# Kernel tuning notes

Hardware: AMD Instinct MI355X
Metric: run time of the kernel (lower is better)

Reference implementation:

```python
import jax, jax.numpy as jnp
import numpy as np

DELTA_V = 0.5
DELTA_D = 1.5
ALPHA = 1.0
BETA = 1.0
GAMMA = 0.001
K = 33  # segment count: id 0 = background, 1..32 = instances (matches fill_max)


def setup_inputs() -> dict:
    key = jax.random.key(0)
    k1, k2 = jax.random.split(key)
    embeddings = jax.random.normal(k1, (8, 16, 512, 512), dtype=jnp.float32)
    instance_masks = jax.random.randint(k2, (8, 512, 512), 0, K, dtype=jnp.int32)
    return {"embeddings": embeddings, "instance_masks": instance_masks}


def _safe_norm(sq):
    # sqrt with zero-safe gradient: returns 0 where sq == 0
    pos = sq > 0
    return jnp.sqrt(jnp.where(pos, sq, 1.0)) * pos.astype(sq.dtype)


def _per_image(emb, mask):
    # emb: (E, H, W), mask: (H, W)
    E = emb.shape[0]
    emb_flat = emb.reshape(E, -1).T            # (N, E)
    ids = mask.reshape(-1)                      # (N,)

    counts = jax.ops.segment_sum(jnp.ones(ids.shape, jnp.float32), ids, num_segments=K)  # (K,)
    sums = jax.ops.segment_sum(emb_flat, ids, num_segments=K)                             # (K, E)
    counts_c = jnp.maximum(counts, 1.0)
    means = sums / counts_c[:, None]            # (K, E)

    present = counts[1:] > 0                    # (K-1,) which instance ids appear
    n_inst = present.sum().astype(jnp.float32)

    # variance (pull) term: per-pixel distance to own instance mean
    diff = emb_flat - means[ids]                # (N, E)
    pix_d = _safe_norm(jnp.sum(diff * diff, axis=1))
    var_term = jnp.maximum(pix_d - DELTA_V, 0.0) ** 2
    var_per = jax.ops.segment_sum(var_term, ids, num_segments=K)[1:]  # drop background seg
    var_loss = jnp.sum(jnp.where(present, var_per / counts_c[1:], 0.0)) / jnp.maximum(n_inst, 1.0)

    # distance (push) term: pairwise centroid distances among present instances
    m = means[1:]                               # (K-1, E)
    dsq = jnp.sum((m[:, None, :] - m[None, :, :]) ** 2, axis=-1)
    dmat = _safe_norm(dsq)
    pair_mask = (jnp.triu(jnp.ones((K - 1, K - 1), bool), 1)
                 & present[:, None] & present[None, :])
    n_pairs = pair_mask.sum().astype(jnp.float32)
    dist_term = jnp.maximum(2.0 * DELTA_D - dmat, 0.0) ** 2
    dist_loss = jnp.sum(jnp.where(pair_mask, dist_term, 0.0)) / jnp.maximum(n_pairs, 1.0)
    dist_loss = dist_loss * (n_inst > 1.0).astype(jnp.float32)

    # regularization: mean centroid norm over present instances
    mean_norms = _safe_norm(jnp.sum(m * m, axis=1))
    reg_loss = jnp.sum(jnp.where(present, mean_norms, 0.0)) / jnp.maximum(n_inst, 1.0)

    valid = (n_inst > 0.0).astype(jnp.float32)
    return var_loss * valid, dist_loss * valid, reg_loss * valid, valid


def reference(embeddings, instance_masks):
    v, d, r, valid = jax.vmap(_per_image)(embeddings, instance_masks)
    vs = jnp.maximum(valid.sum(), 1.0)
    var_loss = v.sum() / vs
    dist_loss = d.sum() / vs
    reg_loss = r.sum() / vs
    total = ALPHA * var_loss + BETA * dist_loss + GAMMA * reg_loss
    return jnp.stack([total, var_loss, dist_loss, reg_loss])
```

## Files before the change

kernel.cpp:

```cpp
#include <hip/hip_runtime.h>
#include <math.h>


#define B 8
#define E 16
#define HW (512*512)
#define BLK 256
#define P1_BPI 128
#define P2_BPI 64
#define P2_VPB (HW / 4 / P2_BPI)

typedef __attribute__((ext_vector_type(8)))  short short8;
typedef __attribute__((ext_vector_type(16))) float floatx16;

__device__ __forceinline__ float atomAddF(float* p, float v) {
  return unsafeAtomicAdd(p, v);
}

__device__ __forceinline__ short f2bf(float f) {
  unsigned u = __float_as_uint(f);
  u = u + 0x7FFF + ((u >> 16) & 1);
  return (short)(u >> 16);
}

__global__ __launch_bounds__(BLK) void pass1_kernel(
    const float* __restrict__ emb, const int* __restrict__ mask,
    float* __restrict__ gsum ) {
  __shared__ float lred[4][32][33];
  const int b    = blockIdx.y;
  const int t    = threadIdx.x;
  const int lane = t & 63;
  const int wv   = __builtin_amdgcn_readfirstlane(t >> 6);
  const int n    = lane & 31;
  const int h    = lane >> 5;
  const int myid = n + 1;

  const int ppw    = HW / (P1_BPI * 4);
  const int base   = (blockIdx.x * 4 + wv) * ppw;
  const int ntiles = ppw / 16;

  const int*   __restrict__ mb = mask + (size_t)b * HW + base;
  const float* __restrict__ pl = emb + ((size_t)b * E + (n & 15)) * HW + base + 8 * h;

  floatx16 acc;
#pragma unroll
  for (int i = 0; i < 16; ++i) acc[i] = 0.f;

#pragma unroll 2
  for (int tl = 0; tl < ntiles; ++tl) {
    const int4 m0 = ((const int4*)(mb + tl * 16))[0];
    const int4 m1 = ((const int4*)(mb + tl * 16))[1];
    const int4 m2 = ((const int4*)(mb + tl * 16))[2];
    const int4 m3 = ((const int4*)(mb + tl * 16))[3];

    short8 bf;
    if (n < 16) {
      const float4 f0 = ((const float4*)(pl + tl * 16))[0];
      const float4 f1 = ((const float4*)(pl + tl * 16))[1];
      bf[0] = f2bf(f0.x); bf[1] = f2bf(f0.y); bf[2] = f2bf(f0.z); bf[3] = f2bf(f0.w);
      bf[4] = f2bf(f1.x); bf[5] = f2bf(f1.y); bf[6] = f2bf(f1.z); bf[7] = f2bf(f1.w);
    } else if (n == 16) {
      const short one = (short)0x3F80;
      bf[0]=one; bf[1]=one; bf[2]=one; bf[3]=one; bf[4]=one; bf[5]=one; bf[6]=one; bf[7]=one;
    } else {
      bf[0]=0; bf[1]=0; bf[2]=0; bf[3]=0; bf[4]=0; bf[5]=0; bf[6]=0; bf[7]=0;
    }

    const int4 ma = h ? m2 : m0;
    const int4 mc = h ? m3 : m1;
    short8 af;
    af[0] = (ma.x == myid) ? (short)0x3F80 : (short)0;
    af[1] = (ma.y == myid) ? (short)0x3F80 : (short)0;
    af[2] = (ma.z == myid) ? (short)0x3F80 : (short)0;
    af[3] = (ma.w == myid) ? (short)0x3F80 : (short)0;
    af[4] = (mc.x == myid) ? (short)0x3F80 : (short)0;
    af[5] = (mc.y == myid) ? (short)0x3F80 : (short)0;
    af[6] = (mc.z == myid) ? (short)0x3F80 : (short)0;
    af[7] = (mc.w == myid) ? (short)0x3F80 : (short)0;

    acc = __builtin_amdgcn_mfma_f32_32x32x16_bf16(af, bf, acc, 0, 0, 0);
  }

#pragma unroll
  for (int r = 0; r < 16; ++r) {
    const int row = (r & 3) + 8 * (r >> 2) + 4 * h;
    lred[wv][row][n] = acc[r];
  }
  __syncthreads();

  for (int i = t; i < 32 * 32; i += BLK) {
    const int row = i >> 5, col = i & 31;
    if (col < 17) {
      const float s = lred[0][row][col] + lred[1][row][col]
                    + lred[2][row][col] + lred[3][row][col];
      atomAddF(&gsum[((size_t)b * 32 + row) * 17 + col], s);
    }
  }
}

__global__ __launch_bounds__(BLK) void pass2_kernel(
    const float* __restrict__ emb, const int* __restrict__ mask,
    const float* __restrict__ gsum, float* __restrict__ var_per ) {
  __shared__ float mean[33][20];
  __shared__ float slots[4][64][33];
  const int b    = blockIdx.y;
  const int t    = threadIdx.x;
  const int lane = t & 63;
  const int wv   = t >> 6;

  for (int i = t; i < 33 * 20; i += BLK) {
    const int k = i / 20, e = i - k * 20;
    float m = 0.f;
    if (k >= 1 && e < E) {
      const float c  = gsum[((size_t)b * 32 + (k - 1)) * 17 + 16];
      const float cc = c > 1.f ? c : 1.f;
      m = gsum[((size_t)b * 32 + (k - 1)) * 17 + e] / cc;
    }
    mean[k][e] = m;
  }
  for (int i = t; i < 4 * 64 * 33; i += BLK) (&slots[0][0][0])[i] = 0.f;
  __syncthreads();

  const int4*  __restrict__ maskv = (const int4*)(mask + (size_t)b * HW);
  const float* __restrict__ embb  = emb + (size_t)b * E * HW;
  float* mys = &slots[wv][lane][0];
  const int v0 = blockIdx.x * P2_VPB;

#pragma unroll 1
  for (int v = v0 + t; v < v0 + P2_VPB; v += BLK) {
    const int4 id = maskv[v];
    float d0 = 0.f, d1 = 0.f, d2 = 0.f, d3 = 0.f;
#pragma unroll
    for (int j = 0; j < 4; ++j) {
      const float4 x0 = ((const float4*)(embb + (size_t)(4 * j + 0) * HW))[v];
      const float4 x1 = ((const float4*)(embb + (size_t)(4 * j + 1) * HW))[v];
      const float4 x2 = ((const float4*)(embb + (size_t)(4 * j + 2) * HW))[v];
      const float4 x3 = ((const float4*)(embb + (size_t)(4 * j + 3) * HW))[v];
      const float4 m0 = *(const float4*)&mean[id.x][4 * j];
      const float4 m1 = *(const float4*)&mean[id.y][4 * j];
      const float4 m2 = *(const float4*)&mean[id.z][4 * j];
      const float4 m3 = *(const float4*)&mean[id.w][4 * j];
      float u;
      u = x0.x - m0.x; d0 += u * u;  u = x1.x - m0.y; d0 += u * u;
      u = x2.x - m0.z; d0 += u * u;  u = x3.x - m0.w; d0 += u * u;
      u = x0.y - m1.x; d1 += u * u;  u = x1.y - m1.y; d1 += u * u;
      u = x2.y - m1.z; d1 += u * u;  u = x3.y - m1.w; d1 += u * u;
      u = x0.z - m2.x; d2 += u * u;  u = x1.z - m2.y; d2 += u * u;
      u = x2.z - m2.z; d2 += u * u;  u = x3.z - m2.w; d2 += u * u;
      u = x0.w - m3.x; d3 += u * u;  u = x1.w - m3.y; d3 += u * u;
      u = x2.w - m3.z; d3 += u * u;  u = x3.w - m3.w; d3 += u * u;
    }
    float hh;
    hh = fmaxf(sqrtf(d0) - 0.5f, 0.f); mys[id.x] += hh * hh;
    hh = fmaxf(sqrtf(d1) - 0.5f, 0.f); mys[id.y] += hh * hh;
    hh = fmaxf(sqrtf(d2) - 0.5f, 0.f); mys[id.z] += hh * hh;
    hh = fmaxf(sqrtf(d3) - 0.5f, 0.f); mys[id.w] += hh * hh;
  }
  __syncthreads();

  for (int i = t; i < 64 * 33; i += BLK) {
    const int l = i / 33, k = i - l * 33;
    slots[0][l][k] += slots[1][l][k] + slots[2][l][k] + slots[3][l][k];
  }
  __syncthreads();
  if (t >= 1 && t < 33) {
    float s = 0.f;
    for (int l = 0; l < 64; ++l) s += slots[0][l][t];
    atomAddF(&var_per[b * 32 + (t - 1)], s);
  }
}

__global__ __launch_bounds__(BLK) void final_kernel(
    const float* __restrict__ gsum, const float* __restrict__ var_per,
    float* __restrict__ out) {
  __shared__ float mean[B][32][E];
  __shared__ float cnts[B][32];
  __shared__ float vb[B], rb[B], db[B], pb[B], nb[B];
  const int t = threadIdx.x;

  if (t < B) { vb[t] = 0.f; rb[t] = 0.f; db[t] = 0.f; pb[t] = 0.f; nb[t] = 0.f; }
  {
    const int bb = t >> 5, k = t & 31;
    const float c  = gsum[((size_t)bb * 32 + k) * 17 + 16];
    const float cc = c > 1.f ? c : 1.f;
    cnts[bb][k] = c;
#pragma unroll
    for (int e = 0; e < E; ++e)
      mean[bb][k][e] = gsum[((size_t)bb * 32 + k) * 17 + e] / cc;
  }
  __syncthreads();

  {
    const int bb = t >> 5, k = t & 31;
    const float c = cnts[bb][k];
    if (c > 0.5f) {
      atomAddF(&nb[bb], 1.f);
      atomAddF(&vb[bb], var_per[bb * 32 + k] / c);
      float sq = 0.f;
#pragma unroll
      for (int e = 0; e < E; ++e) { const float m = mean[bb][k][e]; sq += m * m; }
      atomAddF(&rb[bb], sq > 0.f ? sqrtf(sq) : 0.f);
    }
  }
  __syncthreads();

  for (int idx = t; idx < B * 32 * 32; idx += BLK) {
    const int bb = idx >> 10;
    const int p  = idx & 1023;
    const int i  = p >> 5;
    const int j  = p & 31;
    if (i < j && cnts[bb][i] > 0.5f && cnts[bb][j] > 0.5f) {
      atomAddF(&pb[bb], 1.f);
      float sq = 0.f;
#pragma unroll
      for (int e = 0; e < E; ++e) {
        const float d = mean[bb][i][e] - mean[bb][j][e];
        sq += d * d;
      }
      const float dn = sq > 0.f ? sqrtf(sq) : 0.f;
      const float hh = 3.0f - dn;
      if (hh > 0.f) atomAddF(&db[bb], hh * hh);
    }
  }
  __syncthreads();

  if (t == 0) {
    float sv = 0.f, sd = 0.f, sr = 0.f, svalid = 0.f;
    for (int bb = 0; bb < B; ++bb) {
      const float ni  = nb[bb];
      const float nim = ni > 1.f ? ni : 1.f;
      const float var_b = vb[bb] / nim;
      const float reg_b = rb[bb] / nim;
      const float npm   = pb[bb] > 1.f ? pb[bb] : 1.f;
      const float dist_b = (ni > 1.f) ? (db[bb] / npm) : 0.f;
      const float valid  = ni > 0.f ? 1.f : 0.f;
      sv += var_b * valid;
      sd += dist_b * valid;
      sr += reg_b * valid;
      svalid += valid;
    }
    const float vs = svalid > 1.f ? svalid : 1.f;
    const float var = sv / vs, dist = sd / vs, reg = sr / vs;
    out[0] = var + dist + 0.001f * reg;
    out[1] = var;
    out[2] = dist;
    out[3] = reg;
  }
}

extern "C" void kernel_launch(void* const* d_in, const int* in_sizes, int n_in,
                              void* d_out, int out_size, void* d_ws, size_t ws_size,
                              hipStream_t stream) {
  const float* emb  = (const float*)d_in[0];
  const int*   mask = (const int*)d_in[1];
  float* out = (float*)d_out;

  float* gsum    = (float*)d_ws;
  float* var_per = (float*)((char*)d_ws + (size_t)B * 32 * 17 * 4);

  hipMemsetAsync(d_ws, 0, (size_t)(B * 32 * 17 + B * 32) * 4, stream);

  pass1_kernel<<<dim3(P1_BPI, B), BLK, 0, stream>>>(emb, mask, gsum);
  pass2_kernel<<<dim3(P2_BPI, B), BLK, 0, stream>>>(emb, mask, gsum, var_per);
  final_kernel<<<1, BLK, 0, stream>>>(gsum, var_per, out);
}
```

Measured before the change: 254.9 us.

## Prefetch pass1 tiles, cheaper bf16 pack, and slim pass2 shared reductions

Pass1 now software-prefetches the next tile's mask and embedding loads before doing the current tile's MFMA. It also packs bf16 values by truncation with a perm instruction instead of round-to-nearest, which adds some truncation error to the sums. Pass2 doubles the block count per image and loads all 16 embedding channels up front. It also swizzles the mean table to spread LDS bank accesses and replaces the large per-lane slot arrays with 8-way shared atomics. The smaller LDS footprint and leaner reduction should raise occupancy, but the shared atomics can contend when many pixels share an id.

```diff
diff --git a/kernel.cpp b/kernel.cpp
--- a/kernel.cpp
+++ b/kernel.cpp
@@ -7,7 +7,7 @@
 #define HW (512*512)
 #define BLK 256
 #define P1_BPI 128
-#define P2_BPI 64
+#define P2_BPI 128
 #define P2_VPB (HW / 4 / P2_BPI)
 
 typedef __attribute__((ext_vector_type(8)))  short short8;
@@ -17,10 +17,20 @@
   return unsafeAtomicAdd(p, v);
 }
 
-__device__ __forceinline__ short f2bf(float f) {
-  unsigned u = __float_as_uint(f);
-  u = u + 0x7FFF + ((u >> 16) & 1);
-  return (short)(u >> 16);
+__device__ __forceinline__ unsigned pack_bf(float a, float b) {
+  return __builtin_amdgcn_perm(__float_as_uint(b), __float_as_uint(a), 0x07060302u);
+}
+
+struct Tile { int4 ma, mb_, mc, md; float4 f0, f1; };
+
+__device__ __forceinline__ void load_tile(Tile& T, const int* __restrict__ mb,
+                                          const float* __restrict__ pl, int tl, bool ld_emb) {
+  const int4* mp = (const int4*)(mb + tl * 16);
+  T.ma = mp[0]; T.mb_ = mp[1]; T.mc = mp[2]; T.md = mp[3];
+  if (ld_emb) {
+    T.f0 = ((const float4*)(pl + tl * 16))[0];
+    T.f1 = ((const float4*)(pl + tl * 16))[1];
+  }
 }
 
 __global__ __launch_bounds__(BLK) void pass1_kernel(
@@ -34,6 +44,7 @@
   const int n    = lane & 31;
   const int h    = lane >> 5;
   const int myid = n + 1;
+  const bool ld  = (n < 16);
 
   const int ppw    = HW / (P1_BPI * 4);
   const int base   = (blockIdx.x * 4 + wv) * ppw;
@@ -46,19 +57,21 @@
 #pragma unroll
   for (int i = 0; i < 16; ++i) acc[i] = 0.f;
 
+  Tile cur, nxt;
+  load_tile(cur, mb, pl, 0, ld);
+
 #pragma unroll 2
   for (int tl = 0; tl < ntiles; ++tl) {
-    const int4 m0 = ((const int4*)(mb + tl * 16))[0];
-    const int4 m1 = ((const int4*)(mb + tl * 16))[1];
-    const int4 m2 = ((const int4*)(mb + tl * 16))[2];
-    const int4 m3 = ((const int4*)(mb + tl * 16))[3];
+    if (tl + 1 < ntiles) load_tile(nxt, mb, pl, tl + 1, ld);
 
     short8 bf;
-    if (n < 16) {
-      const float4 f0 = ((const float4*)(pl + tl * 16))[0];
-      const float4 f1 = ((const float4*)(pl + tl * 16))[1];
-      bf[0] = f2bf(f0.x); bf[1] = f2bf(f0.y); bf[2] = f2bf(f0.z); bf[3] = f2bf(f0.w);
-      bf[4] = f2bf(f1.x); bf[5] = f2bf(f1.y); bf[6] = f2bf(f1.z); bf[7] = f2bf(f1.w);
+    if (ld) {
+      union { uint4 u; short8 s; } cv;
+      cv.u.x = pack_bf(cur.f0.x, cur.f0.y);
+      cv.u.y = pack_bf(cur.f0.z, cur.f0.w);
+      cv.u.z = pack_bf(cur.f1.x, cur.f1.y);
+      cv.u.w = pack_bf(cur.f1.z, cur.f1.w);
+      bf = cv.s;
     } else if (n == 16) {
       const short one = (short)0x3F80;
       bf[0]=one; bf[1]=one; bf[2]=one; bf[3]=one; bf[4]=one; bf[5]=one; bf[6]=one; bf[7]=one;
@@ -66,19 +79,20 @@
       bf[0]=0; bf[1]=0; bf[2]=0; bf[3]=0; bf[4]=0; bf[5]=0; bf[6]=0; bf[7]=0;
     }
 
-    const int4 ma = h ? m2 : m0;
-    const int4 mc = h ? m3 : m1;
+    const int4 A0 = h ? cur.mc : cur.ma;
+    const int4 A1 = h ? cur.md : cur.mb_;
     short8 af;
-    af[0] = (ma.x == myid) ? (short)0x3F80 : (short)0;
-    af[1] = (ma.y == myid) ? (short)0x3F80 : (short)0;
-    af[2] = (ma.z == myid) ? (short)0x3F80 : (short)0;
-    af[3] = (ma.w == myid) ? (short)0x3F80 : (short)0;
-    af[4] = (mc.x == myid) ? (short)0x3F80 : (short)0;
-    af[5] = (mc.y == myid) ? (short)0x3F80 : (short)0;
-    af[6] = (mc.z == myid) ? (short)0x3F80 : (short)0;
-    af[7] = (mc.w == myid) ? (short)0x3F80 : (short)0;
+    af[0] = (A0.x == myid) ? (short)0x3F80 : (short)0;
+    af[1] = (A0.y == myid) ? (short)0x3F80 : (short)0;
+    af[2] = (A0.z == myid) ? (short)0x3F80 : (short)0;
+    af[3] = (A0.w == myid) ? (short)0x3F80 : (short)0;
+    af[4] = (A1.x == myid) ? (short)0x3F80 : (short)0;
+    af[5] = (A1.y == myid) ? (short)0x3F80 : (short)0;
+    af[6] = (A1.z == myid) ? (short)0x3F80 : (short)0;
+    af[7] = (A1.w == myid) ? (short)0x3F80 : (short)0;
 
     acc = __builtin_amdgcn_mfma_f32_32x32x16_bf16(af, bf, acc, 0, 0, 0);
+    cur = nxt;
   }
 
 #pragma unroll
@@ -101,71 +115,68 @@
 __global__ __launch_bounds__(BLK) void pass2_kernel(
     const float* __restrict__ emb, const int* __restrict__ mask,
     const float* __restrict__ gsum, float* __restrict__ var_per ) {
-  __shared__ float mean[33][20];
-  __shared__ float slots[4][64][33];
-  const int b    = blockIdx.y;
-  const int t    = threadIdx.x;
-  const int lane = t & 63;
-  const int wv   = t >> 6;
-
-  for (int i = t; i < 33 * 20; i += BLK) {
-    const int k = i / 20, e = i - k * 20;
+  __shared__ float mean4[33][4][4];
+  __shared__ float lvar[33][8];
+  const int b = blockIdx.y;
+  const int t = threadIdx.x;
+  const int c = t & 7;
+
+  for (int i = t; i < 33 * 16; i += BLK) {
+    const int k = i >> 4, e = i & 15;
     float m = 0.f;
-    if (k >= 1 && e < E) {
-      const float c  = gsum[((size_t)b * 32 + (k - 1)) * 17 + 16];
-      const float cc = c > 1.f ? c : 1.f;
+    if (k >= 1) {
+      const float cnt = gsum[((size_t)b * 32 + (k - 1)) * 17 + 16];
+      const float cc  = cnt > 1.f ? cnt : 1.f;
       m = gsum[((size_t)b * 32 + (k - 1)) * 17 + e] / cc;
     }
-    mean[k][e] = m;
-  }
-  for (int i = t; i < 4 * 64 * 33; i += BLK) (&slots[0][0][0])[i] = 0.f;
+    const int j = e >> 2;
+    mean4[k][(j + k) & 3][e & 3] = m;
+  }
+  for (int i = t; i < 33 * 8; i += BLK) (&lvar[0][0])[i] = 0.f;
   __syncthreads();
 
   const int4*  __restrict__ maskv = (const int4*)(mask + (size_t)b * HW);
   const float* __restrict__ embb  = emb + (size_t)b * E * HW;
-  float* mys = &slots[wv][lane][0];
   const int v0 = blockIdx.x * P2_VPB;
 
 #pragma unroll 1
   for (int v = v0 + t; v < v0 + P2_VPB; v += BLK) {
     const int4 id = maskv[v];
+    float4 x[E];
+#pragma unroll
+    for (int e = 0; e < E; ++e) x[e] = ((const float4*)(embb + (size_t)e * HW))[v];
+
     float d0 = 0.f, d1 = 0.f, d2 = 0.f, d3 = 0.f;
 #pragma unroll
     for (int j = 0; j < 4; ++j) {
-      const float4 x0 = ((const float4*)(embb + (size_t)(4 * j + 0) * HW))[v];
-      const float4 x1 = ((const float4*)(embb + (size_t)(4 * j + 1) * HW))[v];
-      const float4 x2 = ((const float4*)(embb + (size_t)(4 * j + 2) * HW))[v];
-      const float4 x3 = ((const float4*)(embb + (size_t)(4 * j + 3) * HW))[v];
-      const float4 m0 = *(const float4*)&mean[id.x][4 * j];
-      const float4 m1 = *(const float4*)&mean[id.y][4 * j];
-      const float4 m2 = *(const float4*)&mean[id.z][4 * j];
-      const float4 m3 = *(const float4*)&mean[id.w][4 * j];
+      const float4 m0 = *(const float4*)&mean4[id.x][(j + id.x) & 3][0];
+      const float4 m1 = *(const float4*)&mean4[id.y][(j + id.y) & 3][0];
+      const float4 m2 = *(const float4*)&mean4[id.z][(j + id.z) & 3][0];
+      const float4 m3 = *(const float4*)&mean4[id.w][(j + id.w) & 3][0];
+      const float4 a0 = x[4 * j + 0], a1 = x[4 * j + 1];
+      const float4 a2 = x[4 * j + 2], a3 = x[4 * j + 3];
       float u;
-      u = x0.x - m0.x; d0 += u * u;  u = x1.x - m0.y; d0 += u * u;
-      u = x2.x - m0.z; d0 += u * u;  u = x3.x - m0.w; d0 += u * u;
-      u = x0.y - m1.x; d1 += u * u;  u = x1.y - m1.y; d1 += u * u;
-      u = x2.y - m1.z; d1 += u * u;  u = x3.y - m1.w; d1 += u * u;
-      u = x0.z - m2.x; d2 += u * u;  u = x1.z - m2.y; d2 += u * u;
-      u = x2.z - m2.z; d2 += u * u;  u = x3.z - m2.w; d2 += u * u;
-      u = x0.w - m3.x; d3 += u * u;  u = x1.w - m3.y; d3 += u * u;
-      u = x2.w - m3.z; d3 += u * u;  u = x3.w - m3.w; d3 += u * u;
+      u = a0.x - m0.x; d0 += u * u;  u = a1.x - m0.y; d0 += u * u;
+      u = a2.x - m0.z; d0 += u * u;  u = a3.x - m0.w; d0 += u * u;
+      u = a0.y - m1.x; d1 += u * u;  u = a1.y - m1.y; d1 += u * u;
+      u = a2.y - m1.z; d1 += u * u;  u = a3.y - m1.w; d1 += u * u;
+      u = a0.z - m2.x; d2 += u * u;  u = a1.z - m2.y; d2 += u * u;
+      u = a2.z - m2.z; d2 += u * u;  u = a3.z - m2.w; d2 += u * u;
+      u = a0.w - m3.x; d3 += u * u;  u = a1.w - m3.y; d3 += u * u;
+      u = a2.w - m3.z; d3 += u * u;  u = a3.w - m3.w; d3 += u * u;
     }
     float hh;
-    hh = fmaxf(sqrtf(d0) - 0.5f, 0.f); mys[id.x] += hh * hh;
-    hh = fmaxf(sqrtf(d1) - 0.5f, 0.f); mys[id.y] += hh * hh;
-    hh = fmaxf(sqrtf(d2) - 0.5f, 0.f); mys[id.z] += hh * hh;
-    hh = fmaxf(sqrtf(d3) - 0.5f, 0.f); mys[id.w] += hh * hh;
-  }
-  __syncthreads();
-
-  for (int i = t; i < 64 * 33; i += BLK) {
-    const int l = i / 33, k = i - l * 33;
-    slots[0][l][k] += slots[1][l][k] + slots[2][l][k] + slots[3][l][k];
-  }
-  __syncthreads();
+    hh = fmaxf(sqrtf(d0) - 0.5f, 0.f); atomAddF(&lvar[id.x][c], hh * hh);
+    hh = fmaxf(sqrtf(d1) - 0.5f, 0.f); atomAddF(&lvar[id.y][c], hh * hh);
+    hh = fmaxf(sqrtf(d2) - 0.5f, 0.f); atomAddF(&lvar[id.z][c], hh * hh);
+    hh = fmaxf(sqrtf(d3) - 0.5f, 0.f); atomAddF(&lvar[id.w][c], hh * hh);
+  }
+  __syncthreads();
+
   if (t >= 1 && t < 33) {
     float s = 0.f;
-    for (int l = 0; l < 64; ++l) s += slots[0][l][t];
+#pragma unroll
+    for (int cc = 0; cc < 8; ++cc) s += lvar[t][cc];
     atomAddF(&var_per[b * 32 + (t - 1)], s);
   }
 }
```

After: 251.7 us. Within noise of the previous version (-1.3%).
